# Kernel optimization log

Hardware: AMD Instinct MI355X
Metric: run time of the kernel (lower is better)

## Reference

```python
import jax, jax.numpy as jnp
import numpy as np

B, N, IN_FT, OUT_FT = 256, 512, 64, 64


def setup_inputs() -> dict:
    key = jax.random.key(0)
    k1, k2, k3 = jax.random.split(key, 3)
    seq = jax.random.normal(k1, (B, N, IN_FT), dtype=jnp.float32)
    adj = jax.random.uniform(k2, (B, N, N), dtype=jnp.float32)
    # Xavier-uniform linear weight [out_ft, in_ft]
    limit = float(np.sqrt(6.0 / (IN_FT + OUT_FT)))
    W = jax.random.uniform(k3, (OUT_FT, IN_FT), dtype=jnp.float32, minval=-limit, maxval=limit)
    bias = jnp.zeros((OUT_FT,), dtype=jnp.float32)  # bias.data.fill_(0.0)
    alpha = jnp.asarray(0.25, dtype=jnp.float32)    # PReLU default single param
    return {"seq": seq, "adj": adj, "W": W, "bias": bias, "alpha": alpha}


def reference(seq, adj, W, bias, alpha):
    # fc: seq @ W.T  -> [B, N, out_ft]
    seq_fts = jnp.einsum('bnf,of->bno', seq, W)
    # dense batched adjacency aggregation: adj @ seq_fts -> [B, N, out_ft]
    out = jnp.einsum('bnm,bmo->bno', adj, seq_fts)
    out = out + bias
    # PReLU with shared alpha
    return jnp.where(out >= 0, out, alpha * out)
```

## Files before the change

kernel.cpp:

```cpp
#include <hip/hip_runtime.h>
#include <hip/hip_bf16.h>


#define BATCH 256
#define NTOK  512
#define INF   64
#define OUTF  64

typedef __attribute__((ext_vector_type(8))) __bf16 bf16x8;
typedef __attribute__((ext_vector_type(4))) __bf16 bf16x4;
typedef __attribute__((ext_vector_type(4))) float  f32x4;

__device__ __forceinline__ bf16x8 load_cvt8(const float* __restrict__ p) {
    float4 lo = *(const float4*)p;
    float4 hi = *(const float4*)(p + 4);
    bf16x8 r;
    r[0] = (__bf16)lo.x; r[1] = (__bf16)lo.y; r[2] = (__bf16)lo.z; r[3] = (__bf16)lo.w;
    r[4] = (__bf16)hi.x; r[5] = (__bf16)hi.y; r[6] = (__bf16)hi.z; r[7] = (__bf16)hi.w;
    return r;
}

__device__ __forceinline__ bf16x8 pack8(float4 lo, float4 hi) {
    bf16x8 r;
    r[0] = (__bf16)lo.x; r[1] = (__bf16)lo.y; r[2] = (__bf16)lo.z; r[3] = (__bf16)lo.w;
    r[4] = (__bf16)hi.x; r[5] = (__bf16)hi.y; r[6] = (__bf16)hi.z; r[7] = (__bf16)hi.w;
    return r;
}

__global__ __launch_bounds__(512, 2) void GCN_fused_kernel(
        const float* __restrict__ seq, const float* __restrict__ adj,
        const float* __restrict__ W, const float* __restrict__ bias,
        const float* __restrict__ alpha_p, float* __restrict__ out) {
    __shared__ float smem[32768];

    int b    = blockIdx.x;
    int tid  = threadIdx.x;
    int wave = tid >> 6;
    int lane = tid & 63;
    int row16 = lane & 15;
    int g     = lane >> 4;
    int c     = wave & 3;
    int mt    = wave >> 2;
    int rs    = row16 & 7;

    __bf16* sft = (__bf16*)smem;
    float* buf0 = smem + 16384;
    float* buf1 = smem;

    const float* gadj = adj + (size_t)b * NTOK * NTOK;

#define GLOAD(RG, rbase) do {                                                  \
    _Pragma("unroll")                                                          \
    for (int i_ = 0; i_ < 8; ++i_) {                                           \
        int idx_ = wave * 8 + i_;                                              \
        (RG)[i_] = *(const f32x4*)(gadj + (size_t)((rbase) + (idx_ >> 1)) * NTOK \
                                   + (idx_ & 1) * 256 + lane * 4);             \
    }                                                                          \
} while (0)

#define DSWRITE(RG, dstf) do {                                                 \
    _Pragma("unroll")                                                          \
    for (int i_ = 0; i_ < 8; ++i_) {                                           \
        int idx_ = wave * 8 + i_;                                              \
        int row_ = idx_ >> 1;                                                  \
        *(f32x4*)((dstf) + idx_ * 256 + ((lane ^ (row_ & 7)) << 2)) = (RG)[i_];\
    }                                                                          \
} while (0)

#define COMPUTE(CIDX, cur) do {                                                \
    f32x4 acc; acc[0] = bv; acc[1] = bv; acc[2] = bv; acc[3] = bv;             \
    int rowb_ = (mt * 16 + row16) * 512;                                       \
    _Pragma("unroll")                                                          \
    for (int ks_ = 0; ks_ < 16; ++ks_) {                                       \
        int s0_ = (ks_ * 8 + g * 2) ^ rs;                                      \
        float4 f0_ = *(const float4*)((cur) + rowb_ + s0_ * 4);                \
        float4 f1_ = *(const float4*)((cur) + rowb_ + (s0_ ^ 1) * 4);          \
        bf16x8 a_ = pack8(f0_, f1_);                                           \
        acc = __builtin_amdgcn_mfma_f32_16x16x32_bf16(a_, bbr[ks_], acc, 0, 0, 0); \
    }                                                                          \
    int m_ = (CIDX) * 32 + mt * 16 + g * 4;                                    \
    float* op_ = out + ((size_t)b * NTOK + m_) * OUTF + orow;                  \
    _Pragma("unroll")                                                          \
    for (int j_ = 0; j_ < 4; ++j_) {                                           \
        float v_ = acc[j_];                                                    \
        op_[(size_t)j_ * OUTF] = (v_ >= 0.f) ? v_ : alphav * v_;               \
    }                                                                          \
} while (0)

    f32x4 ra[8], rb[8];
    GLOAD(ra, 0);
    __builtin_amdgcn_sched_barrier(0);

    {
        int mb = wave * 64;
        bf16x8 wf[4][2];
#pragma unroll
        for (int nt = 0; nt < 4; ++nt)
#pragma unroll
            for (int ks = 0; ks < 2; ++ks)
                wf[nt][ks] = load_cvt8(W + (size_t)(nt * 16 + row16) * INF + ks * 32 + g * 8);

#pragma unroll
        for (int mt2 = 0; mt2 < 4; ++mt2) {
            f32x4 pa[4] = {};
#pragma unroll
            for (int ks = 0; ks < 2; ++ks) {
                bf16x8 af = load_cvt8(seq + ((size_t)b * NTOK + mb + mt2 * 16 + row16) * INF + ks * 32 + g * 8);
#pragma unroll
                for (int nt = 0; nt < 4; ++nt)
                    pa[nt] = __builtin_amdgcn_mfma_f32_16x16x32_bf16(af, wf[nt][ks], pa[nt], 0, 0, 0);
            }
#pragma unroll
            for (int nt = 0; nt < 4; ++nt) {
                int o    = nt * 16 + row16;
                int ktok = mb + mt2 * 16 + g * 4;
                int sw   = (ktok >> 3) ^ (o & 7);
                bf16x4 v;
                v[0] = (__bf16)pa[nt][0]; v[1] = (__bf16)pa[nt][1];
                v[2] = (__bf16)pa[nt][2]; v[3] = (__bf16)pa[nt][3];
                *(bf16x4*)((char*)sft + (size_t)o * 1024 + sw * 16 + (ktok & 7) * 2) = v;
            }
        }
    }
    int orow     = c * 16 + row16;
    float bv     = bias[orow];
    float alphav = alpha_p[0];
    __syncthreads();

    bf16x8 bbr[16];
#pragma unroll
    for (int t = 0; t < 16; ++t) {
        int sw = ((t << 2) + g) ^ rs;
        bbr[t] = *(const bf16x8*)((const char*)sft + (size_t)orow * 1024 + sw * 16);
    }
    __syncthreads();

#pragma unroll 1
    for (int it2 = 0; it2 < 8; ++it2) {
        int e = it2 * 2, o = e + 1;

        GLOAD(rb, o * 32);
        __builtin_amdgcn_sched_barrier(0);
        if (it2 == 0) asm volatile("s_waitcnt vmcnt(8)"  ::: "memory");
        else          asm volatile("s_waitcnt vmcnt(12)" ::: "memory");
        __builtin_amdgcn_sched_barrier(0);
        DSWRITE(ra, buf0);
        asm volatile("s_waitcnt lgkmcnt(0)" ::: "memory");
        __builtin_amdgcn_sched_barrier(0);
        __builtin_amdgcn_s_barrier();
        __builtin_amdgcn_sched_barrier(0);
        COMPUTE(e, buf0);

        if (it2 < 7) GLOAD(ra, (e + 2) * 32);
        __builtin_amdgcn_sched_barrier(0);
        if (it2 < 7) asm volatile("s_waitcnt vmcnt(12)" ::: "memory");
        else         asm volatile("s_waitcnt vmcnt(4)"  ::: "memory");
        __builtin_amdgcn_sched_barrier(0);
        DSWRITE(rb, buf1);
        asm volatile("s_waitcnt lgkmcnt(0)" ::: "memory");
        __builtin_amdgcn_sched_barrier(0);
        __builtin_amdgcn_s_barrier();
        __builtin_amdgcn_sched_barrier(0);
        COMPUTE(o, buf1);
    }
#undef GLOAD
#undef DSWRITE
#undef COMPUTE
}

extern "C" void kernel_launch(void* const* d_in, const int* in_sizes, int n_in,
                              void* d_out, int out_size, void* d_ws, size_t ws_size,
                              hipStream_t stream) {
    const float* seq   = (const float*)d_in[0];
    const float* adj   = (const float*)d_in[1];
    const float* W     = (const float*)d_in[2];
    const float* bias  = (const float*)d_in[3];
    const float* alpha = (const float*)d_in[4];
    float* out = (float*)d_out;

    GCN_fused_kernel<<<dim3(BATCH), dim3(512), 0, stream>>>(seq, adj, W, bias, alpha, out);
}
```

Before: 71.70 us.

## Triple-buffer adjacency register prefetch with distance-two lookahead, fully unrolled

Replaces the two-register-buffer ping-pong loop with three register buffers that rotate through a fully unrolled 16-step schedule. Each global load is issued two tiles ahead, right after the barrier, so more adjacency data is in flight while the MFMA compute runs. The cost is 32 more VGPRs per thread under a launch bound that was already tight, which risks spills or lower occupancy. The hand-written vmcnt thresholds also count output stores, so the code relies on the compiler's own wait insertion for correctness.

```diff
diff --git a/kernel.cpp b/kernel.cpp
--- a/kernel.cpp
+++ b/kernel.cpp
@@ -87,8 +87,22 @@
     }                                                                          \
 } while (0)
 
-    f32x4 ra[8], rb[8];
-    GLOAD(ra, 0);
+#define BODY(CIDX, CUR, GC, DOLOAD, GN, WAITN) do {                            \
+    asm volatile("s_waitcnt vmcnt(" #WAITN ")" ::: "memory");                  \
+    __builtin_amdgcn_sched_barrier(0);                                         \
+    DSWRITE(GC, CUR);                                                          \
+    asm volatile("s_waitcnt lgkmcnt(0)" ::: "memory");                         \
+    __builtin_amdgcn_sched_barrier(0);                                         \
+    __builtin_amdgcn_s_barrier();                                              \
+    __builtin_amdgcn_sched_barrier(0);                                         \
+    if (DOLOAD) { GLOAD(GN, ((CIDX) + 2) * 32); }                              \
+    __builtin_amdgcn_sched_barrier(0);                                         \
+    COMPUTE(CIDX, CUR);                                                        \
+} while (0)
+
+    f32x4 g0[8], g1[8], g2[8];
+    GLOAD(g0, 0);
+    GLOAD(g1, 32);
     __builtin_amdgcn_sched_barrier(0);
 
     {
@@ -135,34 +149,23 @@
     }
     __syncthreads();
 
-#pragma unroll 1
-    for (int it2 = 0; it2 < 8; ++it2) {
-        int e = it2 * 2, o = e + 1;
-
-        GLOAD(rb, o * 32);
-        __builtin_amdgcn_sched_barrier(0);
-        if (it2 == 0) asm volatile("s_waitcnt vmcnt(8)"  ::: "memory");
-        else          asm volatile("s_waitcnt vmcnt(12)" ::: "memory");
-        __builtin_amdgcn_sched_barrier(0);
-        DSWRITE(ra, buf0);
-        asm volatile("s_waitcnt lgkmcnt(0)" ::: "memory");
-        __builtin_amdgcn_sched_barrier(0);
-        __builtin_amdgcn_s_barrier();
-        __builtin_amdgcn_sched_barrier(0);
-        COMPUTE(e, buf0);
-
-        if (it2 < 7) GLOAD(ra, (e + 2) * 32);
-        __builtin_amdgcn_sched_barrier(0);
-        if (it2 < 7) asm volatile("s_waitcnt vmcnt(12)" ::: "memory");
-        else         asm volatile("s_waitcnt vmcnt(4)"  ::: "memory");
-        __builtin_amdgcn_sched_barrier(0);
-        DSWRITE(rb, buf1);
-        asm volatile("s_waitcnt lgkmcnt(0)" ::: "memory");
-        __builtin_amdgcn_sched_barrier(0);
-        __builtin_amdgcn_s_barrier();
-        __builtin_amdgcn_sched_barrier(0);
-        COMPUTE(o, buf1);
-    }
+    BODY( 0, buf0, g0, 1, g2, 16);
+    BODY( 1, buf1, g1, 1, g0, 16);
+    BODY( 2, buf0, g2, 1, g1, 16);
+    BODY( 3, buf1, g0, 1, g2, 16);
+    BODY( 4, buf0, g1, 1, g0, 16);
+    BODY( 5, buf1, g2, 1, g1, 16);
+    BODY( 6, buf0, g0, 1, g2, 16);
+    BODY( 7, buf1, g1, 1, g0, 16);
+    BODY( 8, buf0, g2, 1, g1, 16);
+    BODY( 9, buf1, g0, 1, g2, 16);
+    BODY(10, buf0, g1, 1, g0, 16);
+    BODY(11, buf1, g2, 1, g1, 16);
+    BODY(12, buf0, g0, 1, g2, 16);
+    BODY(13, buf1, g1, 1, g0, 16);
+    BODY(14, buf0, g2, 0, g0, 16);
+    BODY(15, buf1, g0, 0, g0,  8);
+#undef BODY
 #undef GLOAD
 #undef DSWRITE
 #undef COMPUTE
```

After: 70.75 us. Within noise of the previous version (-1.3%).
